# Kernel tuning notes

Hardware: AMD Instinct MI355X
Metric: run time of the kernel (lower is better)

## Reference

```python
import jax, jax.numpy as jnp
import numpy as np

IMAGE_SIZE = 512
MAX_BOXES = 150
SCORE_THRESH = 0.3
IOU_THRESH = 0.1
BATCH = 32
NUM_CLASS = 20


def setup_inputs():
    key = jax.random.key(0)
    k0, k1, k2, k3 = jax.random.split(key, 4)
    ch = 3 * (5 + NUM_CLASS)  # 75
    fm0 = jax.random.normal(k0, (BATCH, 16, 16, ch), jnp.float32)  # stride 32
    fm1 = jax.random.normal(k1, (BATCH, 32, 32, ch), jnp.float32)  # stride 16
    fm2 = jax.random.normal(k2, (BATCH, 64, 64, ch), jnp.float32)  # stride 8
    # 9 (w,h) anchor sizes in pixels, sorted small->large like YOLOv3
    anchors = jnp.sort(jax.random.uniform(k3, (9, 2), jnp.float32, 10.0, 380.0), axis=0)
    return {"fm0": fm0, "fm1": fm1, "fm2": fm2, "anchors": anchors, "CLASS": NUM_CLASS}


def decode_layer(fm, anchors_layer, num_class):
    # fm: [B, gh, gw, 3*(5+C)]; anchors_layer: [3,2] (w,h)
    b, gh, gw, _ = fm.shape
    ratio = jnp.array([IMAGE_SIZE / gh, IMAGE_SIZE / gw], jnp.float32)  # (ry, rx)
    rescaled = anchors_layer / ratio[::-1]  # (w/rx, h/ry)
    fm = fm.reshape(b, gh, gw, 3, 5 + num_class)
    centers = jax.nn.sigmoid(fm[..., :2])
    sizes = fm[..., 2:4]
    conf = fm[..., 4:5]
    prob = fm[..., 5:]
    gx, gy = jnp.meshgrid(jnp.arange(gw), jnp.arange(gh))  # 'xy' indexing, like tf
    offs = jnp.stack([gx, gy], axis=-1).astype(jnp.float32)[None, :, :, None, :]
    centers = (centers + offs) * ratio[::-1]            # to pixel coords
    sizes = jnp.exp(sizes) * rescaled * ratio[::-1]     # to pixel sizes
    N = gh * gw * 3
    boxes = jnp.concatenate([centers, sizes], axis=-1).reshape(b, N, 4)
    return (boxes,
            jax.nn.sigmoid(conf).reshape(b, N, 1),
            jax.nn.sigmoid(prob).reshape(b, N, num_class))


def nms_single(boxes, scores):
    # boxes [N,4] xyxy, scores [N]; returns kept anchor indices [MAX_BOXES] (-1 = empty)
    N = boxes.shape[0]
    neg = jnp.float32(-1e30)
    s = jnp.where(scores > SCORE_THRESH, scores, neg)  # strict > (K.greater)
    order = jnp.argsort(-s)
    sb = boxes[order]
    ss = s[order]
    area = (sb[:, 2] - sb[:, 0]) * (sb[:, 3] - sb[:, 1])

    def body(i, state):
        suppressed, kept = state
        avail = (~suppressed) & (ss > neg)
        pick = jnp.argmax(avail)          # first available in score order
        ok = avail[pick]
        box = sb[pick]
        ix1 = jnp.maximum(box[0], sb[:, 0])
        iy1 = jnp.maximum(box[1], sb[:, 1])
        ix2 = jnp.minimum(box[2], sb[:, 2])
        iy2 = jnp.minimum(box[3], sb[:, 3])
        inter = jnp.maximum(ix2 - ix1, 0.0) * jnp.maximum(iy2 - iy1, 0.0)
        iou = inter / (area[pick] + area - inter)
        suppressed = suppressed | (ok & (iou > IOU_THRESH))  # self-suppresses (iou=1)
        kept = kept.at[i].set(jnp.where(ok, order[pick], -1))
        return suppressed, kept

    init = (jnp.zeros((N,), bool), jnp.full((MAX_BOXES,), -1, jnp.int32))
    _, kept = jax.lax.fori_loop(0, MAX_BOXES, body, init)
    return kept


def nms_image(boxes, cls_scores):
    # boxes [N,4], cls_scores [N,C]
    C = cls_scores.shape[1]
    kept = jax.vmap(nms_single, in_axes=(None, 1))(
        jax.lax.stop_gradient(boxes), jax.lax.stop_gradient(cls_scores))  # [C,150]
    labels = jnp.broadcast_to(jnp.arange(C)[:, None], kept.shape)
    flat_idx = kept.reshape(-1)
    flat_lab = labels.reshape(-1)
    valid = flat_idx >= 0
    safe_idx = jnp.where(valid, flat_idx, 0)
    flat_sc = jnp.where(valid, cls_scores[safe_idx, flat_lab], -1.0)
    top_sc, top_i = jax.lax.top_k(flat_sc, MAX_BOXES)  # global top-k across classes
    sel_idx = flat_idx[top_i]
    sel_lab = flat_lab[top_i]
    sel_ok = top_sc > 0.0  # real scores are > SCORE_THRESH > 0; pads are -1
    out_boxes = jnp.where(sel_ok[:, None], boxes[jnp.where(sel_ok, sel_idx, 0)], -1.0)
    out_scores = jnp.where(sel_ok, top_sc, -1.0)
    out_labels = jnp.where(sel_ok, sel_lab, -1).astype(jnp.int32)
    return out_boxes, out_scores, out_labels


def reference(fm0, fm1, fm2, anchors, CLASS):
    layers = [(fm0, anchors[6:9]), (fm1, anchors[3:6]), (fm2, anchors[0:3])]
    bl, cl, pl = [], [], []
    for fm, anc in layers:
        b, c, p = decode_layer(fm, anc, CLASS)
        bl.append(b); cl.append(c); pl.append(p)
    boxes = jnp.concatenate(bl, axis=1)   # [B,N,4] (cx,cy,w,h)
    conf = jnp.concatenate(cl, axis=1)    # [B,N,1]
    prob = jnp.concatenate(pl, axis=1)    # [B,N,C]
    cx, cy, w, h = boxes[..., 0], boxes[..., 1], boxes[..., 2], boxes[..., 3]
    boxes = jnp.stack([cx - w / 2, cy - h / 2, cx + w / 2, cy + h / 2], axis=-1)
    scores = conf * prob                  # [B,N,C]
    return jax.vmap(nms_image)(boxes, scores)
```

## Files before the change

### kernel.cpp

```cpp
#include <hip/hip_runtime.h>

#define BATCH 32
#define NUM_CLASS 20
#define NTOT 16128
#define N0 768
#define N1 3072
#define MAX_BOXES 150
#define SORT_N 8192
#define CAND_CAP 7600
#define TOPK_N 4096
#define SCORE_THRESH 0.3f
#define IOU_THRESH 0.1f
#define NMS_W 1024
#define TOPK_W 1024

typedef unsigned long long u64;

__device__ __forceinline__ float exp_f32cr(float x) { return (float)exp((double)x); }
__device__ __forceinline__ float sigm(float x) { return 1.0f / (1.0f + exp_f32cr(-x)); }

__device__ __forceinline__ bool iou_rej2(float4 kb, float ka, float4 c4, float carea) {
    float ix1 = fmaxf(kb.x, c4.x), iy1 = fmaxf(kb.y, c4.y);
    float ix2 = fminf(kb.z, c4.z), iy2 = fminf(kb.w, c4.w);
    float inter = fmaxf(ix2 - ix1, 0.0f) * fmaxf(iy2 - iy1, 0.0f);
    return (inter / (ka + carea - inter)) > IOU_THRESH;
}

__device__ __forceinline__ int phys_idx(int i) { return i ^ ((i >> 4) & 0xF); }

template<int VPT>
__device__ __forceinline__ void bitonic_reg_core(u64 (&r)[VPT], u64* lds, int tid, int nthreads) {
    const int N = nthreads * VPT;
    #pragma unroll
    for (int e = 0; e < VPT; ++e) r[e] = lds[phys_idx(tid * VPT + e)];

    for (int k = 2; k <= N; k <<= 1) {
        int j = k >> 1;
        for (; j >= 64 * VPT; j >>= 1) {
            __syncthreads();
            #pragma unroll
            for (int e = 0; e < VPT; ++e) lds[phys_idx(tid * VPT + e)] = r[e];
            __syncthreads();
            #pragma unroll
            for (int e = 0; e < VPT; ++e) {
                int i = tid * VPT + e;
                u64 q = lds[phys_idx(i ^ j)];
                bool takeMin = (((i & k) == 0) == ((i & j) == 0));
                bool less = r[e] < q;
                r[e] = (takeMin == less) ? r[e] : q;
            }
        }
        for (; j >= VPT; j >>= 1) {
            int ld = j / VPT;
            #pragma unroll
            for (int e = 0; e < VPT; ++e) {
                unsigned lo = (unsigned)r[e], hi = (unsigned)(r[e] >> 32);
                lo = (unsigned)__shfl_xor((int)lo, ld);
                hi = (unsigned)__shfl_xor((int)hi, ld);
                u64 q = ((u64)hi << 32) | lo;
                int i = tid * VPT + e;
                bool takeMin = (((i & k) == 0) == ((i & j) == 0));
                bool less = r[e] < q;
                r[e] = (takeMin == less) ? r[e] : q;
            }
        }
        for (; j >= 1; j >>= 1) {
            #pragma unroll
            for (int e = 0; e < VPT; ++e) {
                int p = e ^ j;
                if (p > e) {
                    int i = tid * VPT + e;
                    bool up = ((i & k) == 0);
                    u64 a = r[e], bkey = r[p];
                    if (up ? (a > bkey) : (a < bkey)) { r[e] = bkey; r[p] = a; }
                }
            }
        }
    }
}

__global__ __launch_bounds__(256) void decode_kernel(
    const float* __restrict__ fm0, const float* __restrict__ fm1,
    const float* __restrict__ fm2, const float* __restrict__ anchors,
    float* __restrict__ boxes, float* __restrict__ scores)
{
    int t = blockIdx.x * 256 + threadIdx.x;
    if (t >= BATCH * NTOT) return;
    int b = t / NTOT, n = t % NTOT;
    const float* fm; int g, arow, local;
    if (n < N0)           { fm = fm0; g = 16; arow = 6; local = n; }
    else if (n < N0 + N1) { fm = fm1; g = 32; arow = 3; local = n - N0; }
    else                  { fm = fm2; g = 64; arow = 0; local = n - (N0 + N1); }
    int cell = local / 3, a = local % 3;
    int gy = cell / g, gx = cell % g;
    const float* p = fm + ((size_t)((b * g + gy) * g + gx) * 75 + (size_t)a * 25);
    float s = 512.0f / (float)g;
    float cx = (sigm(p[0]) + (float)gx) * s;
    float cy = (sigm(p[1]) + (float)gy) * s;
    float w = exp_f32cr(p[2]) * anchors[(arow + a) * 2 + 0];
    float h = exp_f32cr(p[3]) * anchors[(arow + a) * 2 + 1];
    float conf = sigm(p[4]);
    float* bo = boxes + (size_t)t * 4;
    bo[0] = cx - w * 0.5f;
    bo[1] = cy - h * 0.5f;
    bo[2] = cx + w * 0.5f;
    bo[3] = cy + h * 0.5f;
    size_t sb = (size_t)b * NUM_CLASS * NTOT + (size_t)n;
    #pragma unroll
    for (int c = 0; c < NUM_CLASS; ++c)
        scores[sb + (size_t)c * NTOT] = conf * sigm(p[5 + c]);
}

__global__ __launch_bounds__(NMS_W) void sort_kernel(
    const float* __restrict__ scores, u64* __restrict__ skeys,
    int* __restrict__ scnt_g)
{
    __shared__ u64 keys[SORT_N];
    __shared__ unsigned scnt_s;

    const int tid = threadIdx.x;
    const int wlane = tid & 63;
    const int bc = blockIdx.x;

    if (tid == 0) scnt_s = 0u;
    __syncthreads();

    const float* sc = scores + (size_t)bc * NTOT;
    for (int n0 = 0; n0 < NTOT; n0 += NMS_W) {
        int n = n0 + tid;
        float s = (n < NTOT) ? sc[n] : -1.0f;
        bool pass = s > SCORE_THRESH;
        u64 m = __ballot(pass);
        unsigned base = 0;
        if (wlane == 0 && m) base = atomicAdd(&scnt_s, (unsigned)__popcll(m));
        base = __shfl(base, 0);
        if (pass) {
            unsigned pos = base + (unsigned)__popcll(m & ((1ull << wlane) - 1ull));
            if (pos < CAND_CAP) {
                unsigned sbits = ~__float_as_uint(s);
                keys[phys_idx((int)pos)] = ((u64)sbits << 32) | (unsigned)n;
            }
        }
    }
    __syncthreads();
    int cnt = (int)scnt_s; if (cnt > CAND_CAP) cnt = CAND_CAP;
    for (int i = cnt + tid; i < SORT_N; i += NMS_W) keys[phys_idx(i)] = ~0ull;
    __syncthreads();

    u64 r[SORT_N / NMS_W];
    bitonic_reg_core<SORT_N / NMS_W>(r, keys, tid, NMS_W);

    u64* ko = skeys + (size_t)bc * SORT_N;
    #pragma unroll
    for (int e = 0; e < SORT_N / NMS_W; ++e)
        ko[tid * (SORT_N / NMS_W) + e] = r[e];
    if (tid == 0) scnt_g[bc] = cnt;
}

__global__ __launch_bounds__(64) void scan_kernel(
    const float* __restrict__ boxes, const u64* __restrict__ skeys,
    const int* __restrict__ scnt_g,
    int* __restrict__ kept_idx, float* __restrict__ kept_score)
{
    __shared__ float4 kept[MAX_BOXES + 8];
    __shared__ float  karea_s[MAX_BOXES + 8];
    const int lane = threadIdx.x;
    const int bc = blockIdx.x;
    const int b  = bc / NUM_CLASS;

    for (int i = lane; i < MAX_BOXES + 8; i += 64) {
        kept[i] = make_float4(1e30f, 1e30f, 1e30f, 1e30f);
        karea_s[i] = 0.0f;
    }
    __syncthreads();

    const u64* keys = skeys + (size_t)bc * SORT_N;
    int cnt = scnt_g[bc]; if (cnt > CAND_CAP) cnt = CAND_CAP;
    const float* bbase = boxes + (size_t)b * NTOT * 4;
    const size_t obase = (size_t)bc * MAX_BOXES;
    int nk = 0;

    u64 key_cur = keys[lane];
    int  cn_cur = (int)(key_cur & 0xffffffffull);
    bool lv_cur = (lane < cnt);
    float4 c4_cur = lv_cur ? *(const float4*)(bbase + (size_t)cn_cur * 4)
                           : make_float4(0.f, 0.f, 0.f, 0.f);

    for (int s0 = 0; s0 < cnt && nk < MAX_BOXES; s0 += 64) {
        u64 key_nxt = keys[s0 + 64 + lane];
        int  cn_nxt = (int)(key_nxt & 0xffffffffull);
        bool lv_nxt = (s0 + 64 + lane) < cnt;
        float4 c4_nxt = lv_nxt ? *(const float4*)(bbase + (size_t)cn_nxt * 4)
                               : make_float4(0.f, 0.f, 0.f, 0.f);

        int state = 1;
        float cs = __uint_as_float(~(unsigned)(key_cur >> 32));
        float carea = (c4_cur.z - c4_cur.x) * (c4_cur.w - c4_cur.y);
        if (lv_cur) {
            state = 0;
            int nk8 = (nk + 7) & ~7;
            for (int kk = 0; kk < nk8; kk += 8) {
                bool rej = false;
                #pragma unroll
                for (int u = 0; u < 8; ++u)
                    rej |= iou_rej2(kept[kk + u], karea_s[kk + u], c4_cur, carea);
                if (rej) { state = 1; break; }
            }
        }
        while (nk < MAX_BOXES) {
            u64 m = __ballot(state == 0);
            if (!m) break;
            int fi = (int)__builtin_ctzll(m);
            float4 kb;
            kb.x = __shfl(c4_cur.x, fi); kb.y = __shfl(c4_cur.y, fi);
            kb.z = __shfl(c4_cur.z, fi); kb.w = __shfl(c4_cur.w, fi);
            int   kn = __shfl(cn_cur, fi);
            float ks = __shfl(cs, fi);
            float ka = __shfl(carea, fi);
            if (lane == 0) {
                kept[nk] = kb;
                karea_s[nk] = ka;
                kept_idx  [obase + nk] = kn;
                kept_score[obase + nk] = ks;
            }
            if (lane == fi) state = 2;
            else if (state == 0 && iou_rej2(kb, ka, c4_cur, carea)) state = 1;
            ++nk;
        }
        key_cur = key_nxt; cn_cur = cn_nxt; lv_cur = lv_nxt; c4_cur = c4_nxt;
        __syncthreads();
    }
    for (int kx = nk + lane; kx < MAX_BOXES; kx += 64) {
        kept_idx  [obase + kx] = -1;
        kept_score[obase + kx] = -1.0f;
    }
}

__global__ __launch_bounds__(TOPK_W) void topk_kernel(
    const float* __restrict__ boxes, const int* __restrict__ kept_idx,
    const float* __restrict__ kept_score, float* __restrict__ out)
{
    __shared__ u64 keys[TOPK_N];
    const int tid = threadIdx.x;
    const int b = blockIdx.x;
    const int FLAT = NUM_CLASS * MAX_BOXES;

    for (int f = tid; f < TOPK_N; f += TOPK_W) {
        u64 key = ~0ull;
        if (f < FLAT) {
            int idx = kept_idx[(size_t)b * FLAT + f];
            float s = (idx >= 0) ? kept_score[(size_t)b * FLAT + f] : -1.0f;
            unsigned u = __float_as_uint(s);
            unsigned mm = (u & 0x80000000u) ? ~u : (u | 0x80000000u);
            key = ((u64)(~mm) << 32) | (unsigned)f;
        }
        keys[phys_idx(f)] = key;
    }
    __syncthreads();

    u64 r[TOPK_N / TOPK_W];
    bitonic_reg_core<TOPK_N / TOPK_W>(r, keys, tid, TOPK_W);

    __syncthreads();
    #pragma unroll
    for (int e = 0; e < TOPK_N / TOPK_W; ++e)
        keys[phys_idx(tid * (TOPK_N / TOPK_W) + e)] = r[e];
    __syncthreads();

    if (tid < MAX_BOXES) {
        u64 key = keys[phys_idx(tid)];
        int f = (int)(key & 0xffffffffull);
        float sc = -1.0f; int idx = -1;
        if (f < FLAT) {
            idx = kept_idx[(size_t)b * FLAT + f];
            if (idx >= 0) sc = kept_score[(size_t)b * FLAT + f];
        }
        bool ok = (idx >= 0) && (sc > 0.0f);
        float bx0 = -1.0f, bx1 = -1.0f, bx2 = -1.0f, bx3 = -1.0f;
        float lab = -1.0f;
        if (ok) {
            const float* bp = boxes + ((size_t)b * NTOT + idx) * 4;
            bx0 = bp[0]; bx1 = bp[1]; bx2 = bp[2]; bx3 = bp[3];
            lab = (float)(f / MAX_BOXES);
        } else {
            sc = -1.0f;
        }
        float* ob = out + ((size_t)b * MAX_BOXES + tid) * 4;
        ob[0] = bx0; ob[1] = bx1; ob[2] = bx2; ob[3] = bx3;
        out[(size_t)BATCH * MAX_BOXES * 4 + (size_t)b * MAX_BOXES + tid] = sc;
        out[(size_t)BATCH * MAX_BOXES * 5 + (size_t)b * MAX_BOXES + tid] = lab;
    }
}

extern "C" void kernel_launch(void* const* d_in, const int* in_sizes, int n_in,
                              void* d_out, int out_size, void* d_ws, size_t ws_size,
                              hipStream_t stream) {
    const float* fm0 = (const float*)d_in[0];
    const float* fm1 = (const float*)d_in[1];
    const float* fm2 = (const float*)d_in[2];
    const float* anchors = (const float*)d_in[3];
    float* out = (float*)d_out;

    float* boxes  = (float*)d_ws;
    float* scores = boxes + (size_t)BATCH * NTOT * 4;
    u64*   skeys  = (u64*)(scores + (size_t)BATCH * NUM_CLASS * NTOT);
    int*   scnt   = (int*)(skeys + (size_t)BATCH * NUM_CLASS * SORT_N);
    int*   kept_idx   = scnt + BATCH * NUM_CLASS;
    float* kept_score = (float*)(kept_idx + (size_t)BATCH * NUM_CLASS * MAX_BOXES);

    int total = BATCH * NTOT;
    decode_kernel<<<(total + 255) / 256, 256, 0, stream>>>(fm0, fm1, fm2, anchors, boxes, scores);
    sort_kernel<<<BATCH * NUM_CLASS, NMS_W, 0, stream>>>(scores, skeys, scnt);
    scan_kernel<<<BATCH * NUM_CLASS, 64, 0, stream>>>(boxes, skeys, scnt, kept_idx, kept_score);
    topk_kernel<<<BATCH, TOPK_W, 0, stream>>>(boxes, kept_idx, kept_score, out);
}
```

Measured before the change: 419.5 us.

## Fuse sort and greedy NMS scan into one kernel via shared memory

Merges the per-class bitonic sort kernel and the single-wavefront NMS scan kernel into one kernel. The sorted keys are written back to LDS instead of global memory, which removes the round trip of the sorted key array and the candidate count plus one launch. The trade-off is that after sorting, 15 of 16 wavefronts exit while one wavefront runs the serial scan, so the 1024-thread block holds its 64KB+ of LDS for the whole scan. That likely lowers how many blocks can overlap compared with the old 64-thread scan kernel. A bounds check on the candidate index was also added.

New measurement: 481.9 us. 14.9% more time.

```diff
diff --git a/kernel.cpp b/kernel.cpp
--- a/kernel.cpp
+++ b/kernel.cpp
@@ -111,17 +111,24 @@
         scores[sb + (size_t)c * NTOT] = conf * sigm(p[5 + c]);
 }
 
-__global__ __launch_bounds__(NMS_W) void sort_kernel(
-    const float* __restrict__ scores, u64* __restrict__ skeys,
-    int* __restrict__ scnt_g)
+__global__ __launch_bounds__(NMS_W, 8) void nms_kernel(
+    const float* __restrict__ boxes, const float* __restrict__ scores,
+    int* __restrict__ kept_idx, float* __restrict__ kept_score)
 {
     __shared__ u64 keys[SORT_N];
+    __shared__ float4 kept4[MAX_BOXES + 8];
+    __shared__ float  karea_s[MAX_BOXES + 8];
     __shared__ unsigned scnt_s;
 
     const int tid = threadIdx.x;
     const int wlane = tid & 63;
     const int bc = blockIdx.x;
-
+    const int b  = bc / NUM_CLASS;
+
+    for (int i = tid; i < MAX_BOXES + 8; i += NMS_W) {
+        kept4[i] = make_float4(1e30f, 1e30f, 1e30f, 1e30f);
+        karea_s[i] = 0.0f;
+    }
     if (tid == 0) scnt_s = 0u;
     __syncthreads();
 
@@ -149,47 +156,29 @@
 
     u64 r[SORT_N / NMS_W];
     bitonic_reg_core<SORT_N / NMS_W>(r, keys, tid, NMS_W);
-
-    u64* ko = skeys + (size_t)bc * SORT_N;
+    __syncthreads();
     #pragma unroll
     for (int e = 0; e < SORT_N / NMS_W; ++e)
-        ko[tid * (SORT_N / NMS_W) + e] = r[e];
-    if (tid == 0) scnt_g[bc] = cnt;
-}
-
-__global__ __launch_bounds__(64) void scan_kernel(
-    const float* __restrict__ boxes, const u64* __restrict__ skeys,
-    const int* __restrict__ scnt_g,
-    int* __restrict__ kept_idx, float* __restrict__ kept_score)
-{
-    __shared__ float4 kept[MAX_BOXES + 8];
-    __shared__ float  karea_s[MAX_BOXES + 8];
-    const int lane = threadIdx.x;
-    const int bc = blockIdx.x;
-    const int b  = bc / NUM_CLASS;
-
-    for (int i = lane; i < MAX_BOXES + 8; i += 64) {
-        kept[i] = make_float4(1e30f, 1e30f, 1e30f, 1e30f);
-        karea_s[i] = 0.0f;
-    }
-    __syncthreads();
-
-    const u64* keys = skeys + (size_t)bc * SORT_N;
-    int cnt = scnt_g[bc]; if (cnt > CAND_CAP) cnt = CAND_CAP;
+        keys[phys_idx(tid * (SORT_N / NMS_W) + e)] = r[e];
+    __syncthreads();
+
+    if (tid >= 64) return;
+
+    const int lane = tid;
     const float* bbase = boxes + (size_t)b * NTOT * 4;
     const size_t obase = (size_t)bc * MAX_BOXES;
     int nk = 0;
 
-    u64 key_cur = keys[lane];
+    u64 key_cur = keys[phys_idx(lane)];
     int  cn_cur = (int)(key_cur & 0xffffffffull);
-    bool lv_cur = (lane < cnt);
+    bool lv_cur = (lane < cnt) && ((unsigned)cn_cur < (unsigned)NTOT);
     float4 c4_cur = lv_cur ? *(const float4*)(bbase + (size_t)cn_cur * 4)
                            : make_float4(0.f, 0.f, 0.f, 0.f);
 
     for (int s0 = 0; s0 < cnt && nk < MAX_BOXES; s0 += 64) {
-        u64 key_nxt = keys[s0 + 64 + lane];
+        u64 key_nxt = keys[phys_idx(s0 + 64 + lane)];
         int  cn_nxt = (int)(key_nxt & 0xffffffffull);
-        bool lv_nxt = (s0 + 64 + lane) < cnt;
+        bool lv_nxt = ((s0 + 64 + lane) < cnt) && ((unsigned)cn_nxt < (unsigned)NTOT);
         float4 c4_nxt = lv_nxt ? *(const float4*)(bbase + (size_t)cn_nxt * 4)
                                : make_float4(0.f, 0.f, 0.f, 0.f);
 
@@ -203,7 +192,7 @@
                 bool rej = false;
                 #pragma unroll
                 for (int u = 0; u < 8; ++u)
-                    rej |= iou_rej2(kept[kk + u], karea_s[kk + u], c4_cur, carea);
+                    rej |= iou_rej2(kept4[kk + u], karea_s[kk + u], c4_cur, carea);
                 if (rej) { state = 1; break; }
             }
         }
@@ -218,8 +207,7 @@
             float ks = __shfl(cs, fi);
             float ka = __shfl(carea, fi);
             if (lane == 0) {
-                kept[nk] = kb;
-                karea_s[nk] = ka;
+                kept4[nk] = kb; karea_s[nk] = ka;
                 kept_idx  [obase + nk] = kn;
                 kept_score[obase + nk] = ks;
             }
@@ -228,7 +216,7 @@
             ++nk;
         }
         key_cur = key_nxt; cn_cur = cn_nxt; lv_cur = lv_nxt; c4_cur = c4_nxt;
-        __syncthreads();
+        __threadfence_block();
     }
     for (int kx = nk + lane; kx < MAX_BOXES; kx += 64) {
         kept_idx  [obase + kx] = -1;
@@ -303,14 +291,11 @@
 
     float* boxes  = (float*)d_ws;
     float* scores = boxes + (size_t)BATCH * NTOT * 4;
-    u64*   skeys  = (u64*)(scores + (size_t)BATCH * NUM_CLASS * NTOT);
-    int*   scnt   = (int*)(skeys + (size_t)BATCH * NUM_CLASS * SORT_N);
-    int*   kept_idx   = scnt + BATCH * NUM_CLASS;
+    int*   kept_idx   = (int*)(scores + (size_t)BATCH * NUM_CLASS * NTOT);
     float* kept_score = (float*)(kept_idx + (size_t)BATCH * NUM_CLASS * MAX_BOXES);
 
     int total = BATCH * NTOT;
     decode_kernel<<<(total + 255) / 256, 256, 0, stream>>>(fm0, fm1, fm2, anchors, boxes, scores);
-    sort_kernel<<<BATCH * NUM_CLASS, NMS_W, 0, stream>>>(scores, skeys, scnt);
-    scan_kernel<<<BATCH * NUM_CLASS, 64, 0, stream>>>(boxes, skeys, scnt, kept_idx, kept_score);
+    nms_kernel<<<BATCH * NUM_CLASS, NMS_W, 0, stream>>>(boxes, scores, kept_idx, kept_score);
     topk_kernel<<<BATCH, TOPK_W, 0, stream>>>(boxes, kept_idx, kept_score, out);
 }
```

## Widen NMS scan to 256-thread blocks with cross-wave pick via shared memory

Applied to the files above, without the earlier changes.

The greedy NMS scan kernel now uses four wavefronts per class instead of one, so each outer step tests 256 sorted candidates against the kept list in parallel. The next kept box is chosen by taking each wave's lowest ballot bit and the minimum across waves in shared memory. The kept box is then broadcast through LDS instead of lane shuffles. The cost is two block-wide barriers for every kept box, and the prefetch of the next chunk's keys and boxes is dropped.

Measured after the change: 388.4 us. -7.4%, faster.

```diff
diff --git a/kernel.cpp b/kernel.cpp
--- a/kernel.cpp
+++ b/kernel.cpp
@@ -12,6 +12,7 @@
 #define SCORE_THRESH 0.3f
 #define IOU_THRESH 0.1f
 #define NMS_W 1024
+#define SCAN_W 256
 #define TOPK_W 1024
 
 typedef unsigned long long u64;
@@ -157,19 +158,22 @@
     if (tid == 0) scnt_g[bc] = cnt;
 }
 
-__global__ __launch_bounds__(64) void scan_kernel(
+__global__ __launch_bounds__(SCAN_W) void scan_kernel(
     const float* __restrict__ boxes, const u64* __restrict__ skeys,
     const int* __restrict__ scnt_g,
     int* __restrict__ kept_idx, float* __restrict__ kept_score)
 {
-    __shared__ float4 kept[MAX_BOXES + 8];
+    __shared__ float4 kept4[MAX_BOXES + 8];
     __shared__ float  karea_s[MAX_BOXES + 8];
-    const int lane = threadIdx.x;
+    __shared__ int wmin_s[SCAN_W / 64];
+
+    const int tid = threadIdx.x;
+    const int wid = tid >> 6, wlane = tid & 63;
     const int bc = blockIdx.x;
     const int b  = bc / NUM_CLASS;
 
-    for (int i = lane; i < MAX_BOXES + 8; i += 64) {
-        kept[i] = make_float4(1e30f, 1e30f, 1e30f, 1e30f);
+    for (int i = tid; i < MAX_BOXES + 8; i += SCAN_W) {
+        kept4[i] = make_float4(1e30f, 1e30f, 1e30f, 1e30f);
         karea_s[i] = 0.0f;
     }
     __syncthreads();
@@ -180,57 +184,49 @@
     const size_t obase = (size_t)bc * MAX_BOXES;
     int nk = 0;
 
-    u64 key_cur = keys[lane];
-    int  cn_cur = (int)(key_cur & 0xffffffffull);
-    bool lv_cur = (lane < cnt);
-    float4 c4_cur = lv_cur ? *(const float4*)(bbase + (size_t)cn_cur * 4)
-                           : make_float4(0.f, 0.f, 0.f, 0.f);
-
-    for (int s0 = 0; s0 < cnt && nk < MAX_BOXES; s0 += 64) {
-        u64 key_nxt = keys[s0 + 64 + lane];
-        int  cn_nxt = (int)(key_nxt & 0xffffffffull);
-        bool lv_nxt = (s0 + 64 + lane) < cnt;
-        float4 c4_nxt = lv_nxt ? *(const float4*)(bbase + (size_t)cn_nxt * 4)
-                               : make_float4(0.f, 0.f, 0.f, 0.f);
-
-        int state = 1;
-        float cs = __uint_as_float(~(unsigned)(key_cur >> 32));
-        float carea = (c4_cur.z - c4_cur.x) * (c4_cur.w - c4_cur.y);
-        if (lv_cur) {
-            state = 0;
+    for (int s0 = 0; s0 < cnt && nk < MAX_BOXES; s0 += SCAN_W) {
+        int i = s0 + tid;
+        u64 key = keys[i];
+        int cn = (int)(key & 0xffffffffull);
+        bool lv = (i < cnt) && ((unsigned)cn < (unsigned)NTOT);
+        float4 c4 = lv ? *(const float4*)(bbase + (size_t)cn * 4)
+                       : make_float4(0.f, 0.f, 0.f, 0.f);
+        float carea = (c4.z - c4.x) * (c4.w - c4.y);
+        float cs = __uint_as_float(~(unsigned)(key >> 32));
+        int state = lv ? 0 : 1;
+
+        if (state == 0) {
             int nk8 = (nk + 7) & ~7;
             for (int kk = 0; kk < nk8; kk += 8) {
                 bool rej = false;
                 #pragma unroll
                 for (int u = 0; u < 8; ++u)
-                    rej |= iou_rej2(kept[kk + u], karea_s[kk + u], c4_cur, carea);
+                    rej |= iou_rej2(kept4[kk + u], karea_s[kk + u], c4, carea);
                 if (rej) { state = 1; break; }
             }
         }
         while (nk < MAX_BOXES) {
             u64 m = __ballot(state == 0);
-            if (!m) break;
-            int fi = (int)__builtin_ctzll(m);
-            float4 kb;
-            kb.x = __shfl(c4_cur.x, fi); kb.y = __shfl(c4_cur.y, fi);
-            kb.z = __shfl(c4_cur.z, fi); kb.w = __shfl(c4_cur.w, fi);
-            int   kn = __shfl(cn_cur, fi);
-            float ks = __shfl(cs, fi);
-            float ka = __shfl(carea, fi);
-            if (lane == 0) {
-                kept[nk] = kb;
-                karea_s[nk] = ka;
-                kept_idx  [obase + nk] = kn;
-                kept_score[obase + nk] = ks;
-            }
-            if (lane == fi) state = 2;
-            else if (state == 0 && iou_rej2(kb, ka, c4_cur, carea)) state = 1;
+            if (wlane == 0) wmin_s[wid] = m ? (wid * 64 + (int)__builtin_ctzll(m)) : SCAN_W;
+            __syncthreads();
+            int fi = min(min(wmin_s[0], wmin_s[1]), min(wmin_s[2], wmin_s[3]));
+            if (fi >= SCAN_W) break;
+            if (tid == fi) {
+                kept4[nk] = c4; karea_s[nk] = carea;
+                kept_idx  [obase + nk] = cn;
+                kept_score[obase + nk] = cs;
+                state = 2;
+            }
+            __syncthreads();
+            if (state == 0) {
+                float4 kb = kept4[nk]; float ka = karea_s[nk];
+                if (iou_rej2(kb, ka, c4, carea)) state = 1;
+            }
             ++nk;
         }
-        key_cur = key_nxt; cn_cur = cn_nxt; lv_cur = lv_nxt; c4_cur = c4_nxt;
         __syncthreads();
     }
-    for (int kx = nk + lane; kx < MAX_BOXES; kx += 64) {
+    for (int kx = nk + tid; kx < MAX_BOXES; kx += SCAN_W) {
         kept_idx  [obase + kx] = -1;
         kept_score[obase + kx] = -1.0f;
     }
@@ -311,6 +307,6 @@
     int total = BATCH * NTOT;
     decode_kernel<<<(total + 255) / 256, 256, 0, stream>>>(fm0, fm1, fm2, anchors, boxes, scores);
     sort_kernel<<<BATCH * NUM_CLASS, NMS_W, 0, stream>>>(scores, skeys, scnt);
-    scan_kernel<<<BATCH * NUM_CLASS, 64, 0, stream>>>(boxes, skeys, scnt, kept_idx, kept_score);
+    scan_kernel<<<BATCH * NUM_CLASS, SCAN_W, 0, stream>>>(boxes, skeys, scnt, kept_idx, kept_score);
     topk_kernel<<<BATCH, TOPK_W, 0, stream>>>(boxes, kept_idx, kept_score, out);
 }
```
